# Kernel optimization log

Measured on AMD Instinct MI355X. Metric: run time of the kernel, lower is better.

Reference implementation:

```python
import jax, jax.numpy as jnp
import numpy as np

BATCH = 4096
DIM_X = 256


def setup_inputs() -> dict:
    key = jax.random.key(0)
    k1, k2 = jax.random.split(key)
    inputs = jax.random.normal(k1, (BATCH, DIM_X), dtype=jnp.float32)
    # learned density-matrix parameter (original inits to zeros; use small randn
    # so the quadratic form is non-degenerate for testing)
    rho = jax.random.normal(k2, (DIM_X, DIM_X), dtype=jnp.float32) * 0.02
    return {"inputs": inputs, "rho": rho}


def reference(inputs, rho):
    # oper[b,i,k] = x_i * conj(x_k)  -> [B, d, d] outer product per sample
    oper = jnp.einsum('...i,...j->...ij', inputs, jnp.conj(inputs))
    # trace-style double contraction with rho: sum_{i,k,m} oper[b,i,k] rho[k,m] oper[b,m,i]
    # algebraically equals ||x||^2 * (x^H rho x), but computed as in the source.
    rho_res = jnp.einsum('...ik,km,...mi->...', oper, rho, oper)
    return rho_res
```

## Files before the change

kernel.cpp:

```cpp
#include <hip/hip_runtime.h>

#define BATCH 4096
#define DIM   256
#define ROWS  16
#define NWAVES 8
#define KPW   (DIM / NWAVES)

__global__ __launch_bounds__(512, 2) void qmd_kernel(
    const float* __restrict__ X,
    const float* __restrict__ rho,
    float* __restrict__ out)
{
    __shared__ float4 xs4[ROWS][DIM / 4];
    __shared__ float  red_q[ROWS][NWAVES];
    __shared__ float  red_s[ROWS];

    const int tid  = threadIdx.x;
    const int wave = tid >> 6;
    const int lane = tid & 63;
    const int r0   = blockIdx.x * ROWS;

    {
        const float4* Xg = (const float4*)(X + (size_t)r0 * DIM);
        #pragma unroll
        for (int i = 0; i < 2; ++i) {
            int idx = tid + i * 512;
            int r = idx >> 6, c = idx & 63;
            xs4[r][c] = Xg[r * 64 + c];
        }
    }
    __syncthreads();

    float4 acc[ROWS];
    #pragma unroll
    for (int r = 0; r < ROWS; ++r) acc[r] = make_float4(0.f, 0.f, 0.f, 0.f);

    const int kbase = wave * KPW;
    const float4* rho4 = (const float4*)rho;

    for (int kk = 0; kk < KPW; kk += 4) {
        const int k = kbase + kk;
        float4 xr[ROWS];
        #pragma unroll
        for (int r = 0; r < ROWS; ++r) xr[r] = xs4[r][k >> 2];
        #pragma unroll
        for (int j = 0; j < 4; ++j) {
            float4 rv = rho4[(size_t)(k + j) * (DIM / 4) + lane];
            #pragma unroll
            for (int r = 0; r < ROWS; ++r) {
                float xv = (j == 0) ? xr[r].x : (j == 1) ? xr[r].y
                         : (j == 2) ? xr[r].z : xr[r].w;
                acc[r].x += xv * rv.x;
                acc[r].y += xv * rv.y;
                acc[r].z += xv * rv.z;
                acc[r].w += xv * rv.w;
            }
        }
    }

    float qp[ROWS];
    #pragma unroll
    for (int r = 0; r < ROWS; ++r) {
        float4 xv = xs4[r][lane];
        qp[r] = acc[r].x * xv.x + acc[r].y * xv.y + acc[r].z * xv.z + acc[r].w * xv.w;
    }

    #pragma unroll
    for (int r = 0; r < ROWS; ++r) {
        float v = qp[r];
        #pragma unroll
        for (int off = 32; off > 0; off >>= 1)
            v += __shfl_xor(v, off, 64);
        if (lane == 0) red_q[r][wave] = v;
    }

    if (wave == 0) {
        #pragma unroll
        for (int r = 0; r < ROWS; ++r) {
            float4 xv = xs4[r][lane];
            float v = xv.x * xv.x + xv.y * xv.y + xv.z * xv.z + xv.w * xv.w;
            #pragma unroll
            for (int off = 32; off > 0; off >>= 1)
                v += __shfl_xor(v, off, 64);
            if (lane == 0) red_s[r] = v;
        }
    }
    __syncthreads();

    if (tid < ROWS) {
        float q = 0.f;
        #pragma unroll
        for (int w = 0; w < NWAVES; ++w) q += red_q[tid][w];
        out[r0 + tid] = q * red_s[tid];
    }
}

extern "C" void kernel_launch(void* const* d_in, const int* in_sizes, int n_in,
                              void* d_out, int out_size, void* d_ws, size_t ws_size,
                              hipStream_t stream) {
    const float* X   = (const float*)d_in[0];
    const float* rho = (const float*)d_in[1];
    float* out = (float*)d_out;
    qmd_kernel<<<BATCH / ROWS, 512, 0, stream>>>(X, rho, out);
}
```

Measured before the change: 68.50 us.

## Compute x^T rho x with bf16 MFMA over 64-row tiles

Replaces the scalar FP32 FMA loop with bf16 MFMA 16x16x32 instructions. X tiles are converted to bf16 into padded shared memory, and rho fragments are loaded from global and converted on the fly. The tile grows to 64 rows per block, so there are fewer blocks and each rho element is reused by more rows. The squared-norm reduction is fused into the load phase. Rounding x and rho to bf16 lowers accuracy, and the epilogue reads X again from global memory.

```diff
diff --git a/kernel.cpp b/kernel.cpp
--- a/kernel.cpp
+++ b/kernel.cpp
@@ -2,95 +2,130 @@
 
 #define BATCH 4096
 #define DIM   256
-#define ROWS  16
-#define NWAVES 8
-#define KPW   (DIM / NWAVES)
+#define ROWS  64
+#define PAD_DIM 264
+
+typedef __attribute__((ext_vector_type(8))) short short8;
+typedef __attribute__((ext_vector_type(4))) float f32x4;
+
+__device__ inline short f32_to_bf16(float f) {
+    union { float f; unsigned u; } v; v.f = f;
+    unsigned r = (v.u + 0x7FFFu + ((v.u >> 16) & 1u)) >> 16;
+    return (short)r;
+}
 
 __global__ __launch_bounds__(512, 2) void qmd_kernel(
     const float* __restrict__ X,
     const float* __restrict__ rho,
     float* __restrict__ out)
 {
-    __shared__ float4 xs4[ROWS][DIM / 4];
-    __shared__ float  red_q[ROWS][NWAVES];
-    __shared__ float  red_s[ROWS];
+    __shared__ unsigned short xbf[ROWS][PAD_DIM];
+    __shared__ float red_q[ROWS][8];
+    __shared__ float red_s[ROWS];
 
     const int tid  = threadIdx.x;
     const int wave = tid >> 6;
     const int lane = tid & 63;
+    const int quad = lane >> 4;
+    const int lrow = lane & 15;
     const int r0   = blockIdx.x * ROWS;
 
     {
-        const float4* Xg = (const float4*)(X + (size_t)r0 * DIM);
+        const int srow = tid >> 3;
+        const int scol = tid & 7;
+        const float4* xrow4 = (const float4*)(X + (size_t)(r0 + srow) * DIM);
+        float s2 = 0.f;
         #pragma unroll
-        for (int i = 0; i < 2; ++i) {
-            int idx = tid + i * 512;
-            int r = idx >> 6, c = idx & 63;
-            xs4[r][c] = Xg[r * 64 + c];
+        for (int j = 0; j < 8; ++j) {
+            float4 v = xrow4[scol + 8 * j];
+            s2 += v.x * v.x + v.y * v.y + v.z * v.z + v.w * v.w;
+            short4 b;
+            b.x = f32_to_bf16(v.x); b.y = f32_to_bf16(v.y);
+            b.z = f32_to_bf16(v.z); b.w = f32_to_bf16(v.w);
+            *(short4*)&xbf[srow][(scol + 8 * j) * 4] = b;
         }
+        s2 += __shfl_xor(s2, 1, 64);
+        s2 += __shfl_xor(s2, 2, 64);
+        s2 += __shfl_xor(s2, 4, 64);
+        if ((tid & 7) == 0) red_s[srow] = s2;
     }
     __syncthreads();
 
-    float4 acc[ROWS];
+    const int kh = wave >> 2;
+    const int ns = wave & 3;
+    const int n_base = ns * 64;
+
+    f32x4 acc[4][4];
     #pragma unroll
-    for (int r = 0; r < ROWS; ++r) acc[r] = make_float4(0.f, 0.f, 0.f, 0.f);
+    for (int m = 0; m < 4; ++m)
+        #pragma unroll
+        for (int n = 0; n < 4; ++n)
+            acc[m][n] = (f32x4){0.f, 0.f, 0.f, 0.f};
 
-    const int kbase = wave * KPW;
-    const float4* rho4 = (const float4*)rho;
+    #pragma unroll
+    for (int ki = 0; ki < 4; ++ki) {
+        const int k0 = (kh * 4 + ki) * 32 + quad * 8;
 
-    for (int kk = 0; kk < KPW; kk += 4) {
-        const int k = kbase + kk;
-        float4 xr[ROWS];
+        short8 afr[4];
         #pragma unroll
-        for (int r = 0; r < ROWS; ++r) xr[r] = xs4[r][k >> 2];
+        for (int mt = 0; mt < 4; ++mt)
+            afr[mt] = *(const short8*)&xbf[mt * 16 + lrow][k0];
+
+        short8 bfr[4];
         #pragma unroll
-        for (int j = 0; j < 4; ++j) {
-            float4 rv = rho4[(size_t)(k + j) * (DIM / 4) + lane];
+        for (int nt = 0; nt < 4; ++nt) {
+            const int n = n_base + nt * 16 + lrow;
+            const float* bp = rho + (size_t)n * DIM + k0;
+            float4 b0 = *(const float4*)bp;
+            float4 b1 = *(const float4*)(bp + 4);
+            short8 b;
+            b[0] = f32_to_bf16(b0.x); b[1] = f32_to_bf16(b0.y);
+            b[2] = f32_to_bf16(b0.z); b[3] = f32_to_bf16(b0.w);
+            b[4] = f32_to_bf16(b1.x); b[5] = f32_to_bf16(b1.y);
+            b[6] = f32_to_bf16(b1.z); b[7] = f32_to_bf16(b1.w);
+            bfr[nt] = b;
+        }
+
+        #pragma unroll
+        for (int mt = 0; mt < 4; ++mt)
             #pragma unroll
-            for (int r = 0; r < ROWS; ++r) {
-                float xv = (j == 0) ? xr[r].x : (j == 1) ? xr[r].y
-                         : (j == 2) ? xr[r].z : xr[r].w;
-                acc[r].x += xv * rv.x;
-                acc[r].y += xv * rv.y;
-                acc[r].z += xv * rv.z;
-                acc[r].w += xv * rv.w;
-            }
-        }
+            for (int nt = 0; nt < 4; ++nt)
+                acc[mt][nt] = __builtin_amdgcn_mfma_f32_16x16x32_bf16(
+                    afr[mt], bfr[nt], acc[mt][nt], 0, 0, 0);
     }
 
-    float qp[ROWS];
+    float qp[4][4];
     #pragma unroll
-    for (int r = 0; r < ROWS; ++r) {
-        float4 xv = xs4[r][lane];
-        qp[r] = acc[r].x * xv.x + acc[r].y * xv.y + acc[r].z * xv.z + acc[r].w * xv.w;
-    }
+    for (int mt = 0; mt < 4; ++mt)
+        #pragma unroll
+        for (int rg = 0; rg < 4; ++rg) {
+            const int row = mt * 16 + quad * 4 + rg;
+            const float* xr = X + (size_t)(r0 + row) * DIM;
+            float q = 0.f;
+            #pragma unroll
+            for (int nt = 0; nt < 4; ++nt)
+                q += acc[mt][nt][rg] * xr[n_base + nt * 16 + lrow];
+            qp[mt][rg] = q;
+        }
 
     #pragma unroll
-    for (int r = 0; r < ROWS; ++r) {
-        float v = qp[r];
+    for (int mt = 0; mt < 4; ++mt)
         #pragma unroll
-        for (int off = 32; off > 0; off >>= 1)
-            v += __shfl_xor(v, off, 64);
-        if (lane == 0) red_q[r][wave] = v;
-    }
-
-    if (wave == 0) {
-        #pragma unroll
-        for (int r = 0; r < ROWS; ++r) {
-            float4 xv = xs4[r][lane];
-            float v = xv.x * xv.x + xv.y * xv.y + xv.z * xv.z + xv.w * xv.w;
-            #pragma unroll
-            for (int off = 32; off > 0; off >>= 1)
-                v += __shfl_xor(v, off, 64);
-            if (lane == 0) red_s[r] = v;
+        for (int rg = 0; rg < 4; ++rg) {
+            float v = qp[mt][rg];
+            v += __shfl_xor(v, 1, 64);
+            v += __shfl_xor(v, 2, 64);
+            v += __shfl_xor(v, 4, 64);
+            v += __shfl_xor(v, 8, 64);
+            if (lrow == 0)
+                red_q[mt * 16 + quad * 4 + rg][wave] = v;
         }
-    }
     __syncthreads();
 
     if (tid < ROWS) {
         float q = 0.f;
         #pragma unroll
-        for (int w = 0; w < NWAVES; ++w) q += red_q[tid][w];
+        for (int w = 0; w < 8; ++w) q += red_q[tid][w];
         out[r0 + tid] = q * red_s[tid];
     }
 }
```

New measurement: 66.21 us. -3.3%, faster.
